# Performance work log

Measured on AMD Instinct MI355X. Metric: run time of the kernel, lower is better.

Reference implementation:

```python
import jax, jax.numpy as jnp
import numpy as np

N, IN_F, OUT_F, EMB = 8192, 256, 128, 16

def setup_inputs() -> dict:
    key = jax.random.key(0)
    ks = jax.random.split(key, 6)
    s_in, s_out = 1.0 / np.sqrt(IN_F), 1.0 / np.sqrt(OUT_F)
    return {
        "h": jax.random.normal(ks[0], (N, IN_F), jnp.float32),
        "eps": jax.random.normal(ks[1], (N, OUT_F), jnp.float32),
        "a_str": jax.random.uniform(ks[2], (N, N), jnp.float32),  # precomputed exp_adj kernel (positive)
        "W_fc": jax.random.normal(ks[3], (IN_F, OUT_F), jnp.float32) * s_in,
        "W_k": jax.random.normal(ks[4], (OUT_F, EMB), jnp.float32) * s_out,
        "W_q": jax.random.normal(ks[5], (OUT_F, EMB), jnp.float32) * s_out,
    }

def reference(h, eps, a_str, W_fc, W_k, W_q):
    # h0 = fc(h); h <- N(0,1) sample (eps) + h0
    hh = eps + h @ W_fc                      # [N, OUT_F]
    k = hh @ W_k                             # [N, EMB]
    q = hh @ W_q                             # [N, EMB]
    a_att = jax.nn.softmax(k @ q.T, axis=-1) # [N, N]
    a = a_str * a_att                        # elementwise structural mask
    a = a / jnp.sum(a, axis=-1, keepdims=True)  # renormalize rows
    return a @ hh                            # [N, OUT_F]
```

## Files before the change

### kernel.cpp

```cpp
#include <hip/hip_runtime.h>
#include <hip/hip_bf16.h>

#define NN     8192
#define INF_   256
#define OF     128
#define EMBD   16
#define JSPLIT 8
#define JCH    (NN / JSPLIT)
#define KV     32
#define NSTEP  (JCH / KV)

typedef __attribute__((ext_vector_type(4)))  float          f32x4;
typedef __attribute__((ext_vector_type(16))) float          f32x16;
typedef __attribute__((ext_vector_type(8)))  short          s16x8;
typedef __attribute__((ext_vector_type(4)))  unsigned int   u32x4;
typedef __attribute__((ext_vector_type(4)))  unsigned short u16x4;

__device__ __forceinline__ unsigned short f2bf(float x) {
  unsigned u = __builtin_bit_cast(unsigned, x);
  return (unsigned short)((u + 0x7FFFu + ((u >> 16) & 1u)) >> 16);
}
__device__ __forceinline__ float bf2f(unsigned short h) {
  return __builtin_bit_cast(float, (unsigned)h << 16);
}
__device__ __forceinline__ float fexp2(float x) {
#if __has_builtin(__builtin_amdgcn_exp2f)
  return __builtin_amdgcn_exp2f(x);
#else
  return exp2f(x);
#endif
}

__global__ __launch_bounds__(256) void k_hh(const float* __restrict__ h,
                                            const float* __restrict__ eps,
                                            const float* __restrict__ Wfc,
                                            float* __restrict__ hh) {
  const int tx = threadIdx.x & 31;
  const int ty = threadIdx.x >> 5;
  const int i0 = blockIdx.x * 16 + ty * 2;
  const int c  = tx * 4;
  f32x4 a0 = *(const f32x4*)&eps[(size_t)i0 * OF + c];
  f32x4 a1 = *(const f32x4*)&eps[(size_t)(i0 + 1) * OF + c];
  const float* h0 = h + (size_t)i0 * INF_;
  const float* h1 = h0 + INF_;
#pragma unroll 2
  for (int kk = 0; kk < INF_; kk += 4) {
    const f32x4 ha = *(const f32x4*)&h0[kk];
    const f32x4 hb = *(const f32x4*)&h1[kk];
#pragma unroll
    for (int u = 0; u < 4; ++u) {
      const f32x4 wv = *(const f32x4*)&Wfc[(size_t)(kk + u) * OF + c];
      a0 += ha[u] * wv;
      a1 += hb[u] * wv;
    }
  }
  *(f32x4*)&hh[(size_t)i0 * OF + c]       = a0;
  *(f32x4*)&hh[(size_t)(i0 + 1) * OF + c] = a1;
}

__global__ __launch_bounds__(256) void k_kq(const float* __restrict__ hh,
                                            const float* __restrict__ Wk,
                                            const float* __restrict__ Wq,
                                            unsigned short* __restrict__ kph,
                                            unsigned short* __restrict__ kpl,
                                            unsigned short* __restrict__ qph,
                                            unsigned short* __restrict__ qpl) {
  const int t   = blockIdx.x * 256 + threadIdx.x;
  const int i   = t >> 3;
  const int sub = t & 7;
  const float* W = (sub < 4) ? Wk : Wq;
  const int e    = (sub & 3) * 4;
  const float* hr = hh + (size_t)i * OF;
  f32x4 acc = {0.f, 0.f, 0.f, 0.f};
#pragma unroll 4
  for (int o = 0; o < OF; o += 4) {
    const f32x4 hv = *(const f32x4*)&hr[o];
#pragma unroll
    for (int u = 0; u < 4; ++u) {
      const f32x4 wv = *(const f32x4*)&W[(size_t)(o + u) * EMBD + e];
      acc += hv[u] * wv;
    }
  }
  if (sub < 4) acc *= 1.4426950408889634f;
  u16x4 hi4, lo4;
#pragma unroll
  for (int u = 0; u < 4; ++u) {
    const unsigned short hb = f2bf(acc[u]);
    hi4[u] = hb;
    lo4[u] = f2bf(acc[u] - bf2f(hb));
  }
  unsigned short* dh = (sub < 4) ? kph : qph;
  unsigned short* dl = (sub < 4) ? kpl : qpl;
  *(u16x4*)&dh[(size_t)i * EMBD + e] = hi4;
  *(u16x4*)&dl[(size_t)i * EMBD + e] = lo4;
}

__global__ __launch_bounds__(256) void k_tr(const float* __restrict__ hh,
                                            short* __restrict__ hhT) {
  __shared__ float tile[64][65];
  const int i0 = blockIdx.x * 64;
  const int o0 = blockIdx.y * 64;
  const int c = threadIdx.x & 63;
  const int r = threadIdx.x >> 6;
#pragma unroll
  for (int rr = 0; rr < 16; ++rr) {
    const int ii = rr * 4 + r;
    tile[ii][c] = hh[(size_t)(i0 + ii) * OF + o0 + c];
  }
  __syncthreads();
#pragma unroll
  for (int rr = 0; rr < 16; ++rr) {
    const int oo = rr * 4 + r;
    hhT[(size_t)(o0 + oo) * NN + i0 + c] = (short)f2bf(tile[c][oo]);
  }
}

__global__ __launch_bounds__(256, 2) void k_attn(
    const float* __restrict__ Astr,
    const unsigned short* __restrict__ kph,
    const unsigned short* __restrict__ kpl,
    const unsigned short* __restrict__ qph,
    const unsigned short* __restrict__ qpl,
    const short* __restrict__ hhT,
    float* __restrict__ accP,
    float* __restrict__ dP) {
  const int tid = threadIdx.x;
  const int l   = tid & 63;
  const int hi  = l >> 5;
  const int m   = l & 31;
  const int wid = blockIdx.x * 4 + (tid >> 6);
  const int p   = wid >> 8;
  const int qr  = (wid & 255) * 32;
  const int j0  = p * JCH;
  const int jperm = (m & 19) | ((m & 8) >> 1) | ((m & 4) << 1);

  const s16x8 kh = *(const s16x8*)(kph + (size_t)(qr + m) * EMBD + hi * 8);
  const s16x8 kl = *(const s16x8*)(kpl + (size_t)(qr + m) * EMBD + hi * 8);

  const float* ap          = Astr + (size_t)(qr + m) * NN + j0 + hi * 8;
  const unsigned short* qhb = qph + (size_t)(j0 + jperm) * EMBD + hi * 8;
  const unsigned short* qlb = qpl + (size_t)(j0 + jperm) * EMBD + hi * 8;
  const short* hp0 = hhT + (size_t)m * NN + j0 + hi * 8;
  const short* hp1 = hp0 + (size_t)32 * NN;
  const short* hp2 = hp0 + (size_t)64 * NN;
  const short* hp3 = hp0 + (size_t)96 * NN;

  f32x16 acc0 = {}, acc1 = {}, acc2 = {}, acc3 = {};
  float dpart = 0.f;

  f32x4 aA[4], aB[4];
  aA[0] = *(const f32x4*)(ap + 0);  aA[1] = *(const f32x4*)(ap + 4);
  aA[2] = *(const f32x4*)(ap + 16); aA[3] = *(const f32x4*)(ap + 20);
  aB[0] = *(const f32x4*)(ap + 32); aB[1] = *(const f32x4*)(ap + 36);
  aB[2] = *(const f32x4*)(ap + 48); aB[3] = *(const f32x4*)(ap + 52);

  auto STEP = [&](int rel, f32x4 (&ac)[4], int rel2) {
    const size_t qo = (size_t)rel * EMBD;
    const s16x8 qh = *(const s16x8*)(qhb + qo);
    const s16x8 ql = *(const s16x8*)(qlb + qo);
    const s16x8 B00 = *(const s16x8*)(hp0 + rel);
    const s16x8 B01 = *(const s16x8*)(hp0 + rel + 16);
    const s16x8 B10 = *(const s16x8*)(hp1 + rel);
    const s16x8 B11 = *(const s16x8*)(hp1 + rel + 16);
    const s16x8 B20 = *(const s16x8*)(hp2 + rel);
    const s16x8 B21 = *(const s16x8*)(hp2 + rel + 16);
    const s16x8 B30 = *(const s16x8*)(hp3 + rel);
    const s16x8 B31 = *(const s16x8*)(hp3 + rel + 16);
    f32x16 sc = {};
    sc = __builtin_amdgcn_mfma_f32_32x32x16_bf16(qh, kh, sc, 0, 0, 0);
    sc = __builtin_amdgcn_mfma_f32_32x32x16_bf16(qh, kl, sc, 0, 0, 0);
    sc = __builtin_amdgcn_mfma_f32_32x32x16_bf16(ql, kh, sc, 0, 0, 0);
    float w[16];
    float d0 = 0.f, d1 = 0.f, d2 = 0.f, d3 = 0.f;
#pragma unroll
    for (int r = 0; r < 16; ++r) {
      const float wv = ac[r >> 2][r & 3] * fexp2(sc[r] - 32.0f);
      w[r] = wv;
      if ((r & 3) == 0) d0 += wv; else if ((r & 3) == 1) d1 += wv;
      else if ((r & 3) == 2) d2 += wv; else d3 += wv;
    }
    dpart += (d0 + d1) + (d2 + d3);
    unsigned int pk[8];
#pragma unroll
    for (int d = 0; d < 8; ++d) {
      pk[d] = (unsigned int)f2bf(w[2 * d]) |
              ((unsigned int)f2bf(w[2 * d + 1]) << 16);
    }
    const float* app = ap + rel2;
    ac[0] = *(const f32x4*)(app);      ac[1] = *(const f32x4*)(app + 4);
    ac[2] = *(const f32x4*)(app + 16); ac[3] = *(const f32x4*)(app + 20);
    const s16x8 A1 = __builtin_bit_cast(s16x8, (u32x4){pk[0], pk[1], pk[2], pk[3]});
    const s16x8 A2 = __builtin_bit_cast(s16x8, (u32x4){pk[4], pk[5], pk[6], pk[7]});
    acc0 = __builtin_amdgcn_mfma_f32_32x32x16_bf16(A1, B00, acc0, 0, 0, 0);
    acc0 = __builtin_amdgcn_mfma_f32_32x32x16_bf16(A2, B01, acc0, 0, 0, 0);
    acc1 = __builtin_amdgcn_mfma_f32_32x32x16_bf16(A1, B10, acc1, 0, 0, 0);
    acc1 = __builtin_amdgcn_mfma_f32_32x32x16_bf16(A2, B11, acc1, 0, 0, 0);
    acc2 = __builtin_amdgcn_mfma_f32_32x32x16_bf16(A1, B20, acc2, 0, 0, 0);
    acc2 = __builtin_amdgcn_mfma_f32_32x32x16_bf16(A2, B21, acc2, 0, 0, 0);
    acc3 = __builtin_amdgcn_mfma_f32_32x32x16_bf16(A1, B30, acc3, 0, 0, 0);
    acc3 = __builtin_amdgcn_mfma_f32_32x32x16_bf16(A2, B31, acc3, 0, 0, 0);
  };

  for (int tt = 0; tt < NSTEP; tt += 2) {
    STEP(tt * KV,       aA, ((tt + 2) & (NSTEP - 1)) * KV);
    STEP((tt + 1) * KV, aB, ((tt + 3) & (NSTEP - 1)) * KV);
  }

  float dd = dpart + __shfl_xor(dpart, 32);
  if (hi == 0) dP[(size_t)p * NN + qr + m] = dd;

#pragma unroll
  for (int r = 0; r < 16; ++r) {
    const int row = (r & 3) + 8 * (r >> 2) + 4 * hi;
    float* o = accP + ((size_t)p * NN + qr + row) * OF + m;
    o[0]  = acc0[r];
    o[32] = acc1[r];
    o[64] = acc2[r];
    o[96] = acc3[r];
  }
}

__global__ __launch_bounds__(256) void k_comb(const float* __restrict__ accP,
                                              const float* __restrict__ dP,
                                              float* __restrict__ out) {
  const int idx = blockIdx.x * 256 + threadIdx.x;
  const int row = idx >> 5;
  const int cq  = (idx & 31) * 4;
  float D = 0.f;
  f32x4 s = {0.f, 0.f, 0.f, 0.f};
#pragma unroll
  for (int pp = 0; pp < JSPLIT; ++pp) {
    D += dP[(size_t)pp * NN + row];
    s += *(const f32x4*)&accP[((size_t)pp * NN + row) * OF + cq];
  }
  *(f32x4*)&out[(size_t)row * OF + cq] = s * (1.0f / D);
}

extern "C" void kernel_launch(void* const* d_in, const int* in_sizes, int n_in,
                              void* d_out, int out_size, void* d_ws, size_t ws_size,
                              hipStream_t stream) {
  const float* h   = (const float*)d_in[0];
  const float* eps = (const float*)d_in[1];
  const float* As  = (const float*)d_in[2];
  const float* Wfc = (const float*)d_in[3];
  const float* Wk  = (const float*)d_in[4];
  const float* Wq  = (const float*)d_in[5];
  float* out = (float*)d_out;

  char* ws = (char*)d_ws;
  unsigned short* kph = (unsigned short*)(ws);
  unsigned short* kpl = (unsigned short*)(ws + (256u << 10));
  unsigned short* qph = (unsigned short*)(ws + (512u << 10));
  unsigned short* qpl = (unsigned short*)(ws + (768u << 10));
  short* hhT  = (short*)(ws + (1u << 20));
  float* hh   = (float*)(ws + (3u << 20));
  float* accP = (float*)(ws + (3u << 20));
  float* dP   = (float*)(ws + (35u << 20));

  k_hh<<<NN / 16, 256, 0, stream>>>(h, eps, Wfc, hh);
  k_kq<<<(NN * 8) / 256, 256, 0, stream>>>(hh, Wk, Wq, kph, kpl, qph, qpl);
  k_tr<<<dim3(NN / 64, OF / 64), 256, 0, stream>>>(hh, hhT);
  k_attn<<<(NN / 32) * JSPLIT / 4, 256, 0, stream>>>(As, kph, kpl, qph, qpl, hhT, accP, dP);
  k_comb<<<(NN * OF / 4) / 256, 256, 0, stream>>>(accP, dP, out);
}
```

Measured before the change: 497.7 us.

## Double key split and reduce partials with atomics instead of a combine pass

Raises the key-dimension split from 8 to 16 so k_attn launches twice as many waves. Each wave now atomically adds its partial numerator and denominator into one zeroed accumulator, replacing per-split partial buffers and the multi-pass combine kernel with a zero kernel plus a simple divide. This aims to improve occupancy and cut the partial-buffer write and read traffic, at the cost of float atomic contention and non-deterministic summation order.

Result: faster. 485.2 us (-2.5%).

```diff
diff --git a/kernel.cpp b/kernel.cpp
--- a/kernel.cpp
+++ b/kernel.cpp
@@ -5,7 +5,7 @@
 #define INF_   256
 #define OF     128
 #define EMBD   16
-#define JSPLIT 8
+#define JSPLIT 16
 #define JCH    (NN / JSPLIT)
 #define KV     32
 #define NSTEP  (JCH / KV)
@@ -29,6 +29,11 @@
 #else
   return exp2f(x);
 #endif
+}
+
+__global__ __launch_bounds__(256) void k_zero(float* __restrict__ z) {
+  const int i = blockIdx.x * 256 + threadIdx.x;
+  *(f32x4*)&z[(size_t)i * 4] = (f32x4){0.f, 0.f, 0.f, 0.f};
 }
 
 __global__ __launch_bounds__(256) void k_hh(const float* __restrict__ h,
@@ -122,8 +127,8 @@
     const unsigned short* __restrict__ qph,
     const unsigned short* __restrict__ qpl,
     const short* __restrict__ hhT,
-    float* __restrict__ accP,
-    float* __restrict__ dP) {
+    float* __restrict__ accS,
+    float* __restrict__ dS) {
   const int tid = threadIdx.x;
   const int l   = tid & 63;
   const int hi  = l >> 5;
@@ -207,33 +212,27 @@
   }
 
   float dd = dpart + __shfl_xor(dpart, 32);
-  if (hi == 0) dP[(size_t)p * NN + qr + m] = dd;
+  if (hi == 0) atomicAdd(&dS[qr + m], dd);
 
 #pragma unroll
   for (int r = 0; r < 16; ++r) {
     const int row = (r & 3) + 8 * (r >> 2) + 4 * hi;
-    float* o = accP + ((size_t)p * NN + qr + row) * OF + m;
-    o[0]  = acc0[r];
-    o[32] = acc1[r];
-    o[64] = acc2[r];
-    o[96] = acc3[r];
-  }
-}
-
-__global__ __launch_bounds__(256) void k_comb(const float* __restrict__ accP,
-                                              const float* __restrict__ dP,
-                                              float* __restrict__ out) {
+    float* o = accS + (size_t)(qr + row) * OF + m;
+    atomicAdd(o + 0,  acc0[r]);
+    atomicAdd(o + 32, acc1[r]);
+    atomicAdd(o + 64, acc2[r]);
+    atomicAdd(o + 96, acc3[r]);
+  }
+}
+
+__global__ __launch_bounds__(256) void k_div(const float* __restrict__ accS,
+                                             const float* __restrict__ dS,
+                                             float* __restrict__ out) {
   const int idx = blockIdx.x * 256 + threadIdx.x;
   const int row = idx >> 5;
   const int cq  = (idx & 31) * 4;
-  float D = 0.f;
-  f32x4 s = {0.f, 0.f, 0.f, 0.f};
-#pragma unroll
-  for (int pp = 0; pp < JSPLIT; ++pp) {
-    D += dP[(size_t)pp * NN + row];
-    s += *(const f32x4*)&accP[((size_t)pp * NN + row) * OF + cq];
-  }
-  *(f32x4*)&out[(size_t)row * OF + cq] = s * (1.0f / D);
+  const f32x4 s = *(const f32x4*)&accS[(size_t)row * OF + cq];
+  *(f32x4*)&out[(size_t)row * OF + cq] = s * (1.0f / dS[row]);
 }
 
 extern "C" void kernel_launch(void* const* d_in, const int* in_sizes, int n_in,
@@ -254,12 +253,13 @@
   unsigned short* qpl = (unsigned short*)(ws + (768u << 10));
   short* hhT  = (short*)(ws + (1u << 20));
   float* hh   = (float*)(ws + (3u << 20));
-  float* accP = (float*)(ws + (3u << 20));
-  float* dP   = (float*)(ws + (35u << 20));
-
+  float* accS = (float*)(ws + (7u << 20));
+  float* dS   = (float*)(ws + (11u << 20));
+
+  k_zero<<<(NN * OF + NN) / (256 * 4), 256, 0, stream>>>(accS);
   k_hh<<<NN / 16, 256, 0, stream>>>(h, eps, Wfc, hh);
   k_kq<<<(NN * 8) / 256, 256, 0, stream>>>(hh, Wk, Wq, kph, kpl, qph, qpl);
   k_tr<<<dim3(NN / 64, OF / 64), 256, 0, stream>>>(hh, hhT);
-  k_attn<<<(NN / 32) * JSPLIT / 4, 256, 0, stream>>>(As, kph, kpl, qph, qpl, hhT, accP, dP);
-  k_comb<<<(NN * OF / 4) / 256, 256, 0, stream>>>(accP, dP, out);
-}
+  k_attn<<<(NN / 32) * JSPLIT / 4, 256, 0, stream>>>(As, kph, kpl, qph, qpl, hhT, accS, dS);
+  k_div<<<(NN * OF / 4) / 256, 256, 0, stream>>>(accS, dS, out);
+}
```
